# Optimization experiments

Hardware: AMD Instinct MI355X
Metric: run time of the kernel (lower is better)

The kernel has to match this reference:

```python
import jax, jax.numpy as jnp
import numpy as np

# SREChead (single level, width=0.25): stem 1x1 (128->64) + two 3x3 convs (64->64),
# each Conv->BN(eval, folded into scale/shift)->SiLU, then 1x1 reg (4ch) and obj (1ch)
# heads, followed by YOLOX-style grid decode.
B, C_IN, HGT, WID = 64, 128, 80, 80
C_H = 64            # int(256 * 0.25)
STRIDE = 32


def _conv(x, w):
    # NCHW conv, stride 1, SAME padding (pad=(k-1)//2 as in BaseConv)
    return jax.lax.conv_general_dilated(
        x, w, window_strides=(1, 1), padding='SAME',
        dimension_numbers=('NCHW', 'OIHW', 'NCHW'))


def _bn_silu(y, scale, shift):
    # eval-mode BatchNorm folded to per-channel affine, then SiLU
    return jax.nn.silu(y * scale[None, :, None, None] + shift[None, :, None, None])


def setup_inputs() -> dict:
    key = jax.random.key(0)
    ks = jax.random.split(key, 12)

    def w(k, o, i, kh, kw, s=0.05):
        return jax.random.normal(k, (o, i, kh, kw), jnp.float32) * s

    def bn(k, c):
        k1, k2 = jax.random.split(k)
        scale = 1.0 + 0.1 * jax.random.normal(k1, (c,), jnp.float32)
        shift = 0.05 * jax.random.normal(k2, (c,), jnp.float32)
        return scale, shift

    stem_scale, stem_shift = bn(ks[2], C_H)
    c1_scale, c1_shift = bn(ks[4], C_H)
    c2_scale, c2_shift = bn(ks[6], C_H)
    return {
        'x': jax.random.normal(ks[0], (B, C_IN, HGT, WID), jnp.float32),
        'stem_w': w(ks[1], C_H, C_IN, 1, 1),
        'stem_scale': stem_scale, 'stem_shift': stem_shift,
        'c1_w': w(ks[3], C_H, C_H, 3, 3),
        'c1_scale': c1_scale, 'c1_shift': c1_shift,
        'c2_w': w(ks[5], C_H, C_H, 3, 3),
        'c2_scale': c2_scale, 'c2_shift': c2_shift,
        'reg_w': w(ks[7], 4, C_H, 1, 1),
        'reg_b': jnp.zeros((4,), jnp.float32),
        'obj_w': w(ks[8], 1, C_H, 1, 1),
        'obj_b': jnp.zeros((1,), jnp.float32),
    }


def reference(x, stem_w, stem_scale, stem_shift,
              c1_w, c1_scale, c1_shift,
              c2_w, c2_scale, c2_shift,
              reg_w, reg_b, obj_w, obj_b):
    f = _bn_silu(_conv(x, stem_w), stem_scale, stem_shift)       # [B,64,H,W]
    f = _bn_silu(_conv(f, c1_w), c1_scale, c1_shift)
    f = _bn_silu(_conv(f, c2_w), c2_scale, c2_shift)
    reg = _conv(f, reg_w) + reg_b[None, :, None, None]           # [B,4,H,W]
    obj = jax.nn.sigmoid(_conv(f, obj_w) + obj_b[None, :, None, None])  # [B,1,H,W]
    out = jnp.concatenate([reg, obj], axis=1)                    # [B,5,H,W]
    out = out.reshape(out.shape[0], 5, HGT * WID).transpose(0, 2, 1)  # [B,HW,5]
    # YOLOX decode: xy = (pred_xy + grid) * stride, wh = exp(pred_wh) * stride
    yv, xv = jnp.meshgrid(jnp.arange(HGT), jnp.arange(WID), indexing='ij')
    grid = jnp.stack([xv, yv], -1).reshape(1, HGT * WID, 2).astype(out.dtype)
    xy = (out[..., :2] + grid) * STRIDE
    wh = jnp.exp(out[..., 2:4]) * STRIDE
    return jnp.concatenate([xy, wh, out[..., 4:5]], axis=-1)     # [B,HW,5]
```

## Files before the change

kernel.cpp:

```cpp
#include <hip/hip_runtime.h>
#include <cstdint>


typedef short short8 __attribute__((ext_vector_type(8)));
typedef float floatx4 __attribute__((ext_vector_type(4)));
typedef float fx4 __attribute__((ext_vector_type(4)));
typedef unsigned short us4 __attribute__((ext_vector_type(4)));

#define NPIX 6400
#define PADIMG (82 * 82 * 64)

static __device__ __forceinline__ unsigned short f2bf(float f) {
    unsigned u = __builtin_bit_cast(unsigned, f);
    u += 0x7fffu + ((u >> 16) & 1u);
    return (unsigned short)(u >> 16);
}

static __device__ __forceinline__ float silu_(float v) {
    return v / (1.0f + __expf(-v));
}

__global__ __launch_bounds__(256) void rearr_w_kernel(
    const float* __restrict__ w1, const float* __restrict__ w2,
    unsigned short* __restrict__ wB1, unsigned short* __restrict__ wB2) {
    int idx = blockIdx.x * 256 + threadIdx.x;
    const float* src = (idx < 36864) ? w1 : w2;
    unsigned short* dst = (idx < 36864) ? wB1 : wB2;
    int e = (idx < 36864) ? idx : idx - 36864;
    int j = e & 7;
    int lane = (e >> 3) & 63;
    int ct = (e >> 9) & 3;
    int kb = e >> 11;
    int co = ct * 16 + (lane & 15);
    int k = kb * 32 + ((lane >> 4) * 8) + j;
    int ci = k & 63;
    int tap = k >> 6;
    dst[e] = f2bf(src[(co * 64 + ci) * 9 + tap]);
}

__global__ __launch_bounds__(256) void border_kernel(
    unsigned short* __restrict__ f1p, unsigned short* __restrict__ f2p) {
    int t = blockIdx.x * 256 + threadIdx.x;
    int chunk = t % 5184;
    int bb = t / 5184;
    int buf = bb >> 6, b = bb & 63;
    int pix = chunk >> 4;
    int c4 = (chunk & 15) * 4;
    int row, col;
    if (pix < 82)       { row = 0;  col = pix; }
    else if (pix < 164) { row = 81; col = pix - 82; }
    else { int j = pix - 164; row = 1 + (j >> 1); col = (j & 1) * 81; }
    unsigned short* base = (buf ? f2p : f1p) + (size_t)b * PADIMG + (row * 82 + col) * 64 + c4;
    us4 z = {0, 0, 0, 0};
    *(us4*)base = z;
}

__global__ __launch_bounds__(256) void stem_kernel(
    const float* __restrict__ x, const float* __restrict__ w,
    const float* __restrict__ scale, const float* __restrict__ shift,
    unsigned short* __restrict__ f1p) {
    int b = blockIdx.y;
    int wv = threadIdx.x >> 6;
    int lane = threadIdx.x & 63;
    int l15 = lane & 15, q = lane >> 4;
    int pbase = blockIdx.x * 256 + wv * 64;

    short8 wf[4][4];
    #pragma unroll
    for (int ct = 0; ct < 4; ++ct) {
        int co = ct * 16 + l15;
        #pragma unroll
        for (int kb = 0; kb < 4; ++kb) {
            const float* wp = w + co * 128 + kb * 32 + q * 8;
            fx4 a = *(const fx4*)wp;
            fx4 bv = *(const fx4*)(wp + 4);
            short8 f;
            #pragma unroll
            for (int j = 0; j < 4; ++j) f[j] = (short)f2bf(a[j]);
            #pragma unroll
            for (int j = 0; j < 4; ++j) f[j + 4] = (short)f2bf(bv[j]);
            wf[ct][kb] = f;
        }
    }
    float sc[4][4], sh[4][4];
    #pragma unroll
    for (int ct = 0; ct < 4; ++ct)
        #pragma unroll
        for (int r = 0; r < 4; ++r) {
            sc[ct][r] = scale[ct * 16 + q * 4 + r];
            sh[ct][r] = shift[ct * 16 + q * 4 + r];
        }

    floatx4 acc[4][4];
    floatx4 zf = {0.0f, 0.0f, 0.0f, 0.0f};
    #pragma unroll
    for (int ct = 0; ct < 4; ++ct)
        #pragma unroll
        for (int pt = 0; pt < 4; ++pt) acc[ct][pt] = zf;

    #pragma unroll
    for (int kb = 0; kb < 4; ++kb) {
        short8 xf[4];
        #pragma unroll
        for (int pt = 0; pt < 4; ++pt) {
            int p = pbase + pt * 16 + l15;
            const float* xp = x + (size_t)(b * 128 + kb * 32 + q * 8) * NPIX + p;
            short8 f;
            #pragma unroll
            for (int j = 0; j < 8; ++j) f[j] = (short)f2bf(xp[j * NPIX]);
            xf[pt] = f;
        }
        #pragma unroll
        for (int ct = 0; ct < 4; ++ct)
            #pragma unroll
            for (int pt = 0; pt < 4; ++pt)
                acc[ct][pt] = __builtin_amdgcn_mfma_f32_16x16x32_bf16(
                    wf[ct][kb], xf[pt], acc[ct][pt], 0, 0, 0);
    }

    #pragma unroll
    for (int pt = 0; pt < 4; ++pt) {
        int p = pbase + pt * 16 + l15;
        int y = p / 80, xc = p % 80;
        unsigned short* dst = f1p + (size_t)b * PADIMG + ((y + 1) * 82 + (xc + 1)) * 64;
        #pragma unroll
        for (int ct = 0; ct < 4; ++ct) {
            us4 v;
            #pragma unroll
            for (int r = 0; r < 4; ++r)
                v[r] = f2bf(silu_(acc[ct][pt][r] * sc[ct][r] + sh[ct][r]));
            *(us4*)(dst + ct * 16 + q * 4) = v;
        }
    }
}

__global__ __launch_bounds__(256, 3) void conv3_kernel(
    const unsigned short* __restrict__ fin, const unsigned short* __restrict__ wB,
    const float* __restrict__ scale, const float* __restrict__ shift,
    unsigned short* __restrict__ fout) {
    int b = blockIdx.y;
    int wv = threadIdx.x >> 6;
    int lane = threadIdx.x & 63;
    int l15 = lane & 15, q = lane >> 4;
    int pbase = blockIdx.x * 256 + wv * 64;

    int py[4], px0[4];
    #pragma unroll
    for (int pt = 0; pt < 4; ++pt) {
        int pt16 = pbase + pt * 16;
        py[pt] = pt16 / 80;
        px0[pt] = pt16 % 80;
    }

    floatx4 acc[4][4];
    floatx4 zf = {0.0f, 0.0f, 0.0f, 0.0f};
    #pragma unroll
    for (int ct = 0; ct < 4; ++ct)
        #pragma unroll
        for (int pt = 0; pt < 4; ++pt) acc[ct][pt] = zf;

    const unsigned short* fb = fin + (size_t)b * PADIMG;

    #pragma unroll
    for (int tap = 0; tap < 9; ++tap) {
        const int dy = tap / 3 - 1, dx = tap % 3 - 1;
        #pragma unroll
        for (int half = 0; half < 2; ++half) {
            const int kb = tap * 2 + half;
            short8 pf[4];
            #pragma unroll
            for (int pt = 0; pt < 4; ++pt) {
                int addr = ((py[pt] + 1 + dy) * 82 + px0[pt] + l15 + 1 + dx) * 64
                         + half * 32 + q * 8;
                pf[pt] = *(const short8*)(fb + addr);
            }
            short8 wf[4];
            #pragma unroll
            for (int ct = 0; ct < 4; ++ct)
                wf[ct] = *(const short8*)(wB + ((kb * 4 + ct) * 64 + lane) * 8);
            #pragma unroll
            for (int ct = 0; ct < 4; ++ct)
                #pragma unroll
                for (int pt = 0; pt < 4; ++pt)
                    acc[ct][pt] = __builtin_amdgcn_mfma_f32_16x16x32_bf16(
                        wf[ct], pf[pt], acc[ct][pt], 0, 0, 0);
        }
    }

    float sc[4][4], sh[4][4];
    #pragma unroll
    for (int ct = 0; ct < 4; ++ct)
        #pragma unroll
        for (int r = 0; r < 4; ++r) {
            sc[ct][r] = scale[ct * 16 + q * 4 + r];
            sh[ct][r] = shift[ct * 16 + q * 4 + r];
        }
    #pragma unroll
    for (int pt = 0; pt < 4; ++pt) {
        unsigned short* dst = fout + (size_t)b * PADIMG
                            + ((py[pt] + 1) * 82 + px0[pt] + l15 + 1) * 64;
        #pragma unroll
        for (int ct = 0; ct < 4; ++ct) {
            us4 v;
            #pragma unroll
            for (int r = 0; r < 4; ++r)
                v[r] = f2bf(silu_(acc[ct][pt][r] * sc[ct][r] + sh[ct][r]));
            *(us4*)(dst + ct * 16 + q * 4) = v;
        }
    }
}

__global__ __launch_bounds__(256, 3) void conv_head_kernel(
    const unsigned short* __restrict__ fin, const unsigned short* __restrict__ wB,
    const float* __restrict__ scale, const float* __restrict__ shift,
    const float* __restrict__ reg_w, const float* __restrict__ reg_b,
    const float* __restrict__ obj_w, const float* __restrict__ obj_b,
    float* __restrict__ out) {
    __shared__ unsigned short h_lds[4][64 * 72];
    int b = blockIdx.y;
    int wv = threadIdx.x >> 6;
    int lane = threadIdx.x & 63;
    int l15 = lane & 15, q = lane >> 4;
    int pbase = blockIdx.x * 256 + wv * 64;

    int py[4], px0[4];
    #pragma unroll
    for (int pt = 0; pt < 4; ++pt) {
        int pt16 = pbase + pt * 16;
        py[pt] = pt16 / 80;
        px0[pt] = pt16 % 80;
    }

    floatx4 acc[4][4];
    floatx4 zf = {0.0f, 0.0f, 0.0f, 0.0f};
    #pragma unroll
    for (int ct = 0; ct < 4; ++ct)
        #pragma unroll
        for (int pt = 0; pt < 4; ++pt) acc[ct][pt] = zf;

    const unsigned short* fb = fin + (size_t)b * PADIMG;

    #pragma unroll
    for (int tap = 0; tap < 9; ++tap) {
        const int dy = tap / 3 - 1, dx = tap % 3 - 1;
        #pragma unroll
        for (int half = 0; half < 2; ++half) {
            const int kb = tap * 2 + half;
            short8 pf[4];
            #pragma unroll
            for (int pt = 0; pt < 4; ++pt) {
                int addr = ((py[pt] + 1 + dy) * 82 + px0[pt] + l15 + 1 + dx) * 64
                         + half * 32 + q * 8;
                pf[pt] = *(const short8*)(fb + addr);
            }
            short8 wf[4];
            #pragma unroll
            for (int ct = 0; ct < 4; ++ct)
                wf[ct] = *(const short8*)(wB + ((kb * 4 + ct) * 64 + lane) * 8);
            #pragma unroll
            for (int ct = 0; ct < 4; ++ct)
                #pragma unroll
                for (int pt = 0; pt < 4; ++pt)
                    acc[ct][pt] = __builtin_amdgcn_mfma_f32_16x16x32_bf16(
                        wf[ct], pf[pt], acc[ct][pt], 0, 0, 0);
        }
    }

    float sc[4][4], sh[4][4];
    #pragma unroll
    for (int ct = 0; ct < 4; ++ct)
        #pragma unroll
        for (int r = 0; r < 4; ++r) {
            sc[ct][r] = scale[ct * 16 + q * 4 + r];
            sh[ct][r] = shift[ct * 16 + q * 4 + r];
        }
    unsigned short* hp = h_lds[wv];
    #pragma unroll
    for (int pt = 0; pt < 4; ++pt) {
        #pragma unroll
        for (int ct = 0; ct < 4; ++ct) {
            us4 v;
            #pragma unroll
            for (int r = 0; r < 4; ++r)
                v[r] = f2bf(silu_(acc[ct][pt][r] * sc[ct][r] + sh[ct][r]));
            *(us4*)(hp + (pt * 16 + l15) * 72 + ct * 16 + q * 4) = v;
        }
    }
    __syncthreads();

    short8 hbf[2];
    #pragma unroll
    for (int kb2 = 0; kb2 < 2; ++kb2) {
        int k0 = kb2 * 32 + q * 8;
        short8 f = {};
        if (l15 < 4) {
            #pragma unroll
            for (int j = 0; j < 8; ++j) f[j] = (short)f2bf(reg_w[l15 * 64 + k0 + j]);
        } else if (l15 == 4) {
            #pragma unroll
            for (int j = 0; j < 8; ++j) f[j] = (short)f2bf(obj_w[k0 + j]);
        }
        hbf[kb2] = f;
    }

    floatx4 acc5[4];
    #pragma unroll
    for (int mt = 0; mt < 4; ++mt) acc5[mt] = zf;
    #pragma unroll
    for (int mt = 0; mt < 4; ++mt)
        #pragma unroll
        for (int kb2 = 0; kb2 < 2; ++kb2) {
            short8 a = *(const short8*)(hp + (mt * 16 + l15) * 72 + kb2 * 32 + q * 8);
            acc5[mt] = __builtin_amdgcn_mfma_f32_16x16x32_bf16(a, hbf[kb2], acc5[mt], 0, 0, 0);
        }

    float bias = 0.0f;
    if (l15 < 4) bias = reg_b[l15];
    else if (l15 == 4) bias = obj_b[0];

    #pragma unroll
    for (int mt = 0; mt < 4; ++mt) {
        #pragma unroll
        for (int r = 0; r < 4; ++r) {
            int p = pbase + mt * 16 + q * 4 + r;
            if (l15 < 5) {
                float v = acc5[mt][r] + bias;
                float gx = (float)(px0[mt] + q * 4 + r);
                float gy = (float)py[mt];
                float o;
                if (l15 == 0)      o = (v + gx) * 32.0f;
                else if (l15 == 1) o = (v + gy) * 32.0f;
                else if (l15 < 4)  o = __expf(v) * 32.0f;
                else               o = 1.0f / (1.0f + __expf(-v));
                out[(size_t)(b * NPIX + p) * 5 + l15] = o;
            }
        }
    }
}

extern "C" void kernel_launch(void* const* d_in, const int* in_sizes, int n_in,
                              void* d_out, int out_size, void* d_ws, size_t ws_size,
                              hipStream_t stream) {
    const float* x          = (const float*)d_in[0];
    const float* stem_w     = (const float*)d_in[1];
    const float* stem_scale = (const float*)d_in[2];
    const float* stem_shift = (const float*)d_in[3];
    const float* c1_w       = (const float*)d_in[4];
    const float* c1_scale   = (const float*)d_in[5];
    const float* c1_shift   = (const float*)d_in[6];
    const float* c2_w       = (const float*)d_in[7];
    const float* c2_scale   = (const float*)d_in[8];
    const float* c2_shift   = (const float*)d_in[9];
    const float* reg_w      = (const float*)d_in[10];
    const float* reg_b      = (const float*)d_in[11];
    const float* obj_w      = (const float*)d_in[12];
    const float* obj_b      = (const float*)d_in[13];
    float* out = (float*)d_out;

    const size_t needed = ((size_t)73728 + 2 * (size_t)64 * PADIMG) * 2;
    if (ws_size < needed) return;

    unsigned short* ws  = (unsigned short*)d_ws;
    unsigned short* wB1 = ws;
    unsigned short* wB2 = ws + 36864;
    unsigned short* f1p = ws + 73728;
    unsigned short* f2p = f1p + (size_t)64 * PADIMG;

    rearr_w_kernel<<<288, 256, 0, stream>>>(c1_w, c2_w, wB1, wB2);
    border_kernel<<<2592, 256, 0, stream>>>(f1p, f2p);
    stem_kernel<<<dim3(25, 64), 256, 0, stream>>>(x, stem_w, stem_scale, stem_shift, f1p);
    conv3_kernel<<<dim3(25, 64), 256, 0, stream>>>(f1p, wB1, c1_scale, c1_shift, f2p);
    conv_head_kernel<<<dim3(25, 64), 256, 0, stream>>>(f2p, wB2, c2_scale, c2_shift,
                                                       reg_w, reg_b, obj_w, obj_b, out);
}
```

Measured before the change: 543.1 us.

## Stage conv halo tiles in LDS, keep weights in registers, drop padded buffers

The 3x3 conv kernels now load a swizzled 6x82 pixel halo tile into shared memory once per block. Each wave holds one 16-channel output slice of weights in registers and loops over 20 pixel tiles, so global re-reads of neighbouring pixels are replaced by LDS reads. The padded intermediate layout and its border-zeroing kernel are removed, with out-of-bounds taps zero-filled during the tile load. The stem kernel now transposes its input through LDS to get coalesced fp32 loads. The costs are a large LDS footprint, more registers (launch bounds lowered to 2 blocks per SM) and a fixed 4-row tiling.

```diff
diff --git a/kernel.cpp b/kernel.cpp
--- a/kernel.cpp
+++ b/kernel.cpp
@@ -8,7 +8,6 @@
 typedef unsigned short us4 __attribute__((ext_vector_type(4)));
 
 #define NPIX 6400
-#define PADIMG (82 * 82 * 64)
 
 static __device__ __forceinline__ unsigned short f2bf(float f) {
     unsigned u = __builtin_bit_cast(unsigned, f);
@@ -38,32 +37,29 @@
     dst[e] = f2bf(src[(co * 64 + ci) * 9 + tap]);
 }
 
-__global__ __launch_bounds__(256) void border_kernel(
-    unsigned short* __restrict__ f1p, unsigned short* __restrict__ f2p) {
-    int t = blockIdx.x * 256 + threadIdx.x;
-    int chunk = t % 5184;
-    int bb = t / 5184;
-    int buf = bb >> 6, b = bb & 63;
-    int pix = chunk >> 4;
-    int c4 = (chunk & 15) * 4;
-    int row, col;
-    if (pix < 82)       { row = 0;  col = pix; }
-    else if (pix < 164) { row = 81; col = pix - 82; }
-    else { int j = pix - 164; row = 1 + (j >> 1); col = (j & 1) * 81; }
-    unsigned short* base = (buf ? f2p : f1p) + (size_t)b * PADIMG + (row * 82 + col) * 64 + c4;
-    us4 z = {0, 0, 0, 0};
-    *(us4*)base = z;
-}
-
 __global__ __launch_bounds__(256) void stem_kernel(
     const float* __restrict__ x, const float* __restrict__ w,
     const float* __restrict__ scale, const float* __restrict__ shift,
-    unsigned short* __restrict__ f1p) {
+    unsigned short* __restrict__ f1) {
+    __shared__ __align__(16) unsigned short xt[128 * 128];
     int b = blockIdx.y;
-    int wv = threadIdx.x >> 6;
-    int lane = threadIdx.x & 63;
+    int tid = threadIdx.x;
+    int pbase = blockIdx.x * 128;
+    int lane = tid & 63, wv = tid >> 6;
     int l15 = lane & 15, q = lane >> 4;
-    int pbase = blockIdx.x * 256 + wv * 64;
+
+    #pragma unroll
+    for (int i = 0; i < 16; ++i) {
+        int ci = i * 8 + (tid >> 5);
+        int pxq = tid & 31;
+        const float* xp = x + ((size_t)b * 128 + ci) * NPIX + pbase + pxq * 4;
+        fx4 v = *(const fx4*)xp;
+        #pragma unroll
+        for (int j = 0; j < 4; ++j) {
+            int px = pxq * 4 + j;
+            xt[px * 128 + (((ci >> 3) ^ (px & 15)) * 8) + (ci & 7)] = f2bf(v[j]);
+        }
+    }
 
     short8 wf[4][4];
     #pragma unroll
@@ -91,202 +87,197 @@
             sh[ct][r] = shift[ct * 16 + q * 4 + r];
         }
 
-    floatx4 acc[4][4];
+    __syncthreads();
+
+    floatx4 acc[4][2];
     floatx4 zf = {0.0f, 0.0f, 0.0f, 0.0f};
     #pragma unroll
     for (int ct = 0; ct < 4; ++ct)
         #pragma unroll
-        for (int pt = 0; pt < 4; ++pt) acc[ct][pt] = zf;
+        for (int t = 0; t < 2; ++t) acc[ct][t] = zf;
 
     #pragma unroll
     for (int kb = 0; kb < 4; ++kb) {
-        short8 xf[4];
-        #pragma unroll
-        for (int pt = 0; pt < 4; ++pt) {
-            int p = pbase + pt * 16 + l15;
-            const float* xp = x + (size_t)(b * 128 + kb * 32 + q * 8) * NPIX + p;
-            short8 f;
-            #pragma unroll
-            for (int j = 0; j < 8; ++j) f[j] = (short)f2bf(xp[j * NPIX]);
-            xf[pt] = f;
+        short8 xf[2];
+        #pragma unroll
+        for (int t = 0; t < 2; ++t) {
+            int px = (wv * 2 + t) * 16 + l15;
+            xf[t] = *(const short8*)(xt + px * 128 + (((kb * 4 + q) ^ (px & 15)) * 8));
         }
         #pragma unroll
         for (int ct = 0; ct < 4; ++ct)
             #pragma unroll
-            for (int pt = 0; pt < 4; ++pt)
-                acc[ct][pt] = __builtin_amdgcn_mfma_f32_16x16x32_bf16(
-                    wf[ct][kb], xf[pt], acc[ct][pt], 0, 0, 0);
-    }
-
-    #pragma unroll
-    for (int pt = 0; pt < 4; ++pt) {
-        int p = pbase + pt * 16 + l15;
-        int y = p / 80, xc = p % 80;
-        unsigned short* dst = f1p + (size_t)b * PADIMG + ((y + 1) * 82 + (xc + 1)) * 64;
+            for (int t = 0; t < 2; ++t)
+                acc[ct][t] = __builtin_amdgcn_mfma_f32_16x16x32_bf16(
+                    wf[ct][kb], xf[t], acc[ct][t], 0, 0, 0);
+    }
+
+    #pragma unroll
+    for (int t = 0; t < 2; ++t) {
+        int pg = pbase + (wv * 2 + t) * 16 + l15;
+        unsigned short* dst = f1 + ((size_t)b * NPIX + pg) * 64;
         #pragma unroll
         for (int ct = 0; ct < 4; ++ct) {
             us4 v;
             #pragma unroll
             for (int r = 0; r < 4; ++r)
-                v[r] = f2bf(silu_(acc[ct][pt][r] * sc[ct][r] + sh[ct][r]));
+                v[r] = f2bf(silu_(acc[ct][t][r] * sc[ct][r] + sh[ct][r]));
             *(us4*)(dst + ct * 16 + q * 4) = v;
         }
     }
 }
 
-__global__ __launch_bounds__(256, 3) void conv3_kernel(
+__global__ __launch_bounds__(256, 2) void conv3_kernel(
     const unsigned short* __restrict__ fin, const unsigned short* __restrict__ wB,
     const float* __restrict__ scale, const float* __restrict__ shift,
     unsigned short* __restrict__ fout) {
+    __shared__ __align__(16) unsigned short tile[492 * 64];
     int b = blockIdx.y;
-    int wv = threadIdx.x >> 6;
-    int lane = threadIdx.x & 63;
+    int y0 = blockIdx.x * 4;
+    int tid = threadIdx.x;
+    int lane = tid & 63, wv = tid >> 6;
     int l15 = lane & 15, q = lane >> 4;
-    int pbase = blockIdx.x * 256 + wv * 64;
-
-    int py[4], px0[4];
-    #pragma unroll
-    for (int pt = 0; pt < 4; ++pt) {
-        int pt16 = pbase + pt * 16;
-        py[pt] = pt16 / 80;
-        px0[pt] = pt16 % 80;
-    }
-
-    floatx4 acc[4][4];
+
+    const unsigned short* fb = fin + (size_t)b * NPIX * 64;
+    #pragma unroll
+    for (int i = 0; i < 16; ++i) {
+        int cid = i * 256 + tid;
+        if (cid < 3936) {
+            int pixL = cid >> 3, chunk = cid & 7;
+            int r = pixL / 82, c = pixL - r * 82;
+            int gy = y0 - 1 + r, gx = c - 1;
+            short8 v = {};
+            if ((unsigned)gy < 80u && (unsigned)gx < 80u)
+                v = *(const short8*)(fb + (size_t)(gy * 80 + gx) * 64 + chunk * 8);
+            *(short8*)(tile + pixL * 64 + ((chunk ^ (pixL & 7)) * 8)) = v;
+        }
+    }
+
+    short8 wreg[18];
+    #pragma unroll
+    for (int kb = 0; kb < 18; ++kb)
+        wreg[kb] = *(const short8*)(wB + ((kb * 4 + wv) * 64 + lane) * 8);
+
+    __syncthreads();
+
+    floatx4 acc[20];
     floatx4 zf = {0.0f, 0.0f, 0.0f, 0.0f};
     #pragma unroll
-    for (int ct = 0; ct < 4; ++ct)
-        #pragma unroll
-        for (int pt = 0; pt < 4; ++pt) acc[ct][pt] = zf;
-
-    const unsigned short* fb = fin + (size_t)b * PADIMG;
+    for (int pt = 0; pt < 20; ++pt) acc[pt] = zf;
 
     #pragma unroll
     for (int tap = 0; tap < 9; ++tap) {
         const int dy = tap / 3 - 1, dx = tap % 3 - 1;
         #pragma unroll
         for (int half = 0; half < 2; ++half) {
-            const int kb = tap * 2 + half;
-            short8 pf[4];
-            #pragma unroll
-            for (int pt = 0; pt < 4; ++pt) {
-                int addr = ((py[pt] + 1 + dy) * 82 + px0[pt] + l15 + 1 + dx) * 64
-                         + half * 32 + q * 8;
-                pf[pt] = *(const short8*)(fb + addr);
+            short8 w8 = wreg[tap * 2 + half];
+            #pragma unroll
+            for (int pt = 0; pt < 20; ++pt) {
+                const int r_o = pt / 5, c_o = (pt % 5) * 16;
+                int pix = (r_o + 1 + dy) * 82 + c_o + l15 + 1 + dx;
+                short8 bf8 = *(const short8*)(
+                    tile + pix * 64 + (((half * 4 + q) ^ (pix & 7)) * 8));
+                acc[pt] = __builtin_amdgcn_mfma_f32_16x16x32_bf16(
+                    w8, bf8, acc[pt], 0, 0, 0);
             }
-            short8 wf[4];
-            #pragma unroll
-            for (int ct = 0; ct < 4; ++ct)
-                wf[ct] = *(const short8*)(wB + ((kb * 4 + ct) * 64 + lane) * 8);
-            #pragma unroll
-            for (int ct = 0; ct < 4; ++ct)
-                #pragma unroll
-                for (int pt = 0; pt < 4; ++pt)
-                    acc[ct][pt] = __builtin_amdgcn_mfma_f32_16x16x32_bf16(
-                        wf[ct], pf[pt], acc[ct][pt], 0, 0, 0);
-        }
-    }
-
-    float sc[4][4], sh[4][4];
-    #pragma unroll
-    for (int ct = 0; ct < 4; ++ct)
-        #pragma unroll
-        for (int r = 0; r < 4; ++r) {
-            sc[ct][r] = scale[ct * 16 + q * 4 + r];
-            sh[ct][r] = shift[ct * 16 + q * 4 + r];
-        }
-    #pragma unroll
-    for (int pt = 0; pt < 4; ++pt) {
-        unsigned short* dst = fout + (size_t)b * PADIMG
-                            + ((py[pt] + 1) * 82 + px0[pt] + l15 + 1) * 64;
-        #pragma unroll
-        for (int ct = 0; ct < 4; ++ct) {
-            us4 v;
-            #pragma unroll
-            for (int r = 0; r < 4; ++r)
-                v[r] = f2bf(silu_(acc[ct][pt][r] * sc[ct][r] + sh[ct][r]));
-            *(us4*)(dst + ct * 16 + q * 4) = v;
-        }
-    }
-}
-
-__global__ __launch_bounds__(256, 3) void conv_head_kernel(
+        }
+    }
+
+    float sc4[4], sh4[4];
+    #pragma unroll
+    for (int r = 0; r < 4; ++r) {
+        sc4[r] = scale[wv * 16 + q * 4 + r];
+        sh4[r] = shift[wv * 16 + q * 4 + r];
+    }
+    #pragma unroll
+    for (int pt = 0; pt < 20; ++pt) {
+        const int r_o = pt / 5, c_o = (pt % 5) * 16;
+        int pg = (y0 + r_o) * 80 + c_o + l15;
+        us4 v;
+        #pragma unroll
+        for (int r = 0; r < 4; ++r)
+            v[r] = f2bf(silu_(acc[pt][r] * sc4[r] + sh4[r]));
+        *(us4*)(fout + ((size_t)b * NPIX + pg) * 64 + wv * 16 + q * 4) = v;
+    }
+}
+
+__global__ __launch_bounds__(256, 2) void conv_head_kernel(
     const unsigned short* __restrict__ fin, const unsigned short* __restrict__ wB,
     const float* __restrict__ scale, const float* __restrict__ shift,
     const float* __restrict__ reg_w, const float* __restrict__ reg_b,
     const float* __restrict__ obj_w, const float* __restrict__ obj_b,
     float* __restrict__ out) {
-    __shared__ unsigned short h_lds[4][64 * 72];
+    __shared__ __align__(16) unsigned short tile[492 * 64];
     int b = blockIdx.y;
-    int wv = threadIdx.x >> 6;
-    int lane = threadIdx.x & 63;
+    int y0 = blockIdx.x * 4;
+    int tid = threadIdx.x;
+    int lane = tid & 63, wv = tid >> 6;
     int l15 = lane & 15, q = lane >> 4;
-    int pbase = blockIdx.x * 256 + wv * 64;
-
-    int py[4], px0[4];
-    #pragma unroll
-    for (int pt = 0; pt < 4; ++pt) {
-        int pt16 = pbase + pt * 16;
-        py[pt] = pt16 / 80;
-        px0[pt] = pt16 % 80;
-    }
-
-    floatx4 acc[4][4];
+
+    const unsigned short* fb = fin + (size_t)b * NPIX * 64;
+    #pragma unroll
+    for (int i = 0; i < 16; ++i) {
+        int cid = i * 256 + tid;
+        if (cid < 3936) {
+            int pixL = cid >> 3, chunk = cid & 7;
+            int r = pixL / 82, c = pixL - r * 82;
+            int gy = y0 - 1 + r, gx = c - 1;
+            short8 v = {};
+            if ((unsigned)gy < 80u && (unsigned)gx < 80u)
+                v = *(const short8*)(fb + (size_t)(gy * 80 + gx) * 64 + chunk * 8);
+            *(short8*)(tile + pixL * 64 + ((chunk ^ (pixL & 7)) * 8)) = v;
+        }
+    }
+
+    short8 wreg[18];
+    #pragma unroll
+    for (int kb = 0; kb < 18; ++kb)
+        wreg[kb] = *(const short8*)(wB + ((kb * 4 + wv) * 64 + lane) * 8);
+
+    __syncthreads();
+
+    floatx4 acc[20];
     floatx4 zf = {0.0f, 0.0f, 0.0f, 0.0f};
     #pragma unroll
-    for (int ct = 0; ct < 4; ++ct)
-        #pragma unroll
-        for (int pt = 0; pt < 4; ++pt) acc[ct][pt] = zf;
-
-    const unsigned short* fb = fin + (size_t)b * PADIMG;
+    for (int pt = 0; pt < 20; ++pt) acc[pt] = zf;
 
     #pragma unroll
     for (int tap = 0; tap < 9; ++tap) {
         const int dy = tap / 3 - 1, dx = tap % 3 - 1;
         #pragma unroll
         for (int half = 0; half < 2; ++half) {
-            const int kb = tap * 2 + half;
-            short8 pf[4];
-            #pragma unroll
-            for (int pt = 0; pt < 4; ++pt) {
-                int addr = ((py[pt] + 1 + dy) * 82 + px0[pt] + l15 + 1 + dx) * 64
-                         + half * 32 + q * 8;
-                pf[pt] = *(const short8*)(fb + addr);
+            short8 w8 = wreg[tap * 2 + half];
+            #pragma unroll
+            for (int pt = 0; pt < 20; ++pt) {
+                const int r_o = pt / 5, c_o = (pt % 5) * 16;
+                int pix = (r_o + 1 + dy) * 82 + c_o + l15 + 1 + dx;
+                short8 bf8 = *(const short8*)(
+                    tile + pix * 64 + (((half * 4 + q) ^ (pix & 7)) * 8));
+                acc[pt] = __builtin_amdgcn_mfma_f32_16x16x32_bf16(
+                    w8, bf8, acc[pt], 0, 0, 0);
             }
-            short8 wf[4];
-            #pragma unroll
-            for (int ct = 0; ct < 4; ++ct)
-                wf[ct] = *(const short8*)(wB + ((kb * 4 + ct) * 64 + lane) * 8);
-            #pragma unroll
-            for (int ct = 0; ct < 4; ++ct)
-                #pragma unroll
-                for (int pt = 0; pt < 4; ++pt)
-                    acc[ct][pt] = __builtin_amdgcn_mfma_f32_16x16x32_bf16(
-                        wf[ct], pf[pt], acc[ct][pt], 0, 0, 0);
-        }
-    }
-
-    float sc[4][4], sh[4][4];
-    #pragma unroll
-    for (int ct = 0; ct < 4; ++ct)
-        #pragma unroll
-        for (int r = 0; r < 4; ++r) {
-            sc[ct][r] = scale[ct * 16 + q * 4 + r];
-            sh[ct][r] = shift[ct * 16 + q * 4 + r];
-        }
-    unsigned short* hp = h_lds[wv];
-    #pragma unroll
-    for (int pt = 0; pt < 4; ++pt) {
-        #pragma unroll
-        for (int ct = 0; ct < 4; ++ct) {
-            us4 v;
-            #pragma unroll
-            for (int r = 0; r < 4; ++r)
-                v[r] = f2bf(silu_(acc[ct][pt][r] * sc[ct][r] + sh[ct][r]));
-            *(us4*)(hp + (pt * 16 + l15) * 72 + ct * 16 + q * 4) = v;
-        }
-    }
-    __syncthreads();
+        }
+    }
+
+    __syncthreads();
+
+    float sc4[4], sh4[4];
+    #pragma unroll
+    for (int r = 0; r < 4; ++r) {
+        sc4[r] = scale[wv * 16 + q * 4 + r];
+        sh4[r] = shift[wv * 16 + q * 4 + r];
+    }
+    int gco = (wv * 2 + (q >> 1));
+    #pragma unroll
+    for (int pt = 0; pt < 20; ++pt) {
+        const int r_o = pt / 5, c_o = (pt % 5) * 16;
+        int pix = r_o * 80 + c_o + l15;
+        us4 v;
+        #pragma unroll
+        for (int r = 0; r < 4; ++r)
+            v[r] = f2bf(silu_(acc[pt][r] * sc4[r] + sh4[r]));
+        *(us4*)(tile + pix * 64 + ((gco ^ (pix & 7)) * 8) + (q & 1) * 4) = v;
+    }
 
     short8 hbf[2];
     #pragma unroll
@@ -303,36 +294,44 @@
         hbf[kb2] = f;
     }
 
-    floatx4 acc5[4];
-    #pragma unroll
-    for (int mt = 0; mt < 4; ++mt) acc5[mt] = zf;
-    #pragma unroll
-    for (int mt = 0; mt < 4; ++mt)
+    __syncthreads();
+
+    floatx4 acc5[5];
+    #pragma unroll
+    for (int t = 0; t < 5; ++t) acc5[t] = zf;
+    #pragma unroll
+    for (int t = 0; t < 5; ++t) {
+        int mt = wv * 5 + t;
         #pragma unroll
         for (int kb2 = 0; kb2 < 2; ++kb2) {
-            short8 a = *(const short8*)(hp + (mt * 16 + l15) * 72 + kb2 * 32 + q * 8);
-            acc5[mt] = __builtin_amdgcn_mfma_f32_16x16x32_bf16(a, hbf[kb2], acc5[mt], 0, 0, 0);
-        }
+            int pix = mt * 16 + l15;
+            short8 a = *(const short8*)(
+                tile + pix * 64 + (((kb2 * 4 + q) ^ (pix & 7)) * 8));
+            acc5[t] = __builtin_amdgcn_mfma_f32_16x16x32_bf16(
+                a, hbf[kb2], acc5[t], 0, 0, 0);
+        }
+    }
 
     float bias = 0.0f;
     if (l15 < 4) bias = reg_b[l15];
     else if (l15 == 4) bias = obj_b[0];
 
     #pragma unroll
-    for (int mt = 0; mt < 4; ++mt) {
+    for (int t = 0; t < 5; ++t) {
+        int mt = wv * 5 + t;
         #pragma unroll
         for (int r = 0; r < 4; ++r) {
-            int p = pbase + mt * 16 + q * 4 + r;
+            int pixL = mt * 16 + q * 4 + r;
             if (l15 < 5) {
-                float v = acc5[mt][r] + bias;
-                float gx = (float)(px0[mt] + q * 4 + r);
-                float gy = (float)py[mt];
+                float v = acc5[t][r] + bias;
+                float gx = (float)(pixL % 80);
+                float gy = (float)(y0 + pixL / 80);
                 float o;
                 if (l15 == 0)      o = (v + gx) * 32.0f;
                 else if (l15 == 1) o = (v + gy) * 32.0f;
                 else if (l15 < 4)  o = __expf(v) * 32.0f;
                 else               o = 1.0f / (1.0f + __expf(-v));
-                out[(size_t)(b * NPIX + p) * 5 + l15] = o;
+                out[((size_t)b * NPIX + y0 * 80 + pixL) * 5 + l15] = o;
             }
         }
     }
@@ -357,19 +356,18 @@
     const float* obj_b      = (const float*)d_in[13];
     float* out = (float*)d_out;
 
-    const size_t needed = ((size_t)73728 + 2 * (size_t)64 * PADIMG) * 2;
+    const size_t needed = ((size_t)73728 + 2 * (size_t)64 * NPIX * 64) * 2;
     if (ws_size < needed) return;
 
     unsigned short* ws  = (unsigned short*)d_ws;
     unsigned short* wB1 = ws;
     unsigned short* wB2 = ws + 36864;
-    unsigned short* f1p = ws + 73728;
-    unsigned short* f2p = f1p + (size_t)64 * PADIMG;
+    unsigned short* f1  = ws + 73728;
+    unsigned short* f2  = f1 + (size_t)64 * NPIX * 64;
 
     rearr_w_kernel<<<288, 256, 0, stream>>>(c1_w, c2_w, wB1, wB2);
-    border_kernel<<<2592, 256, 0, stream>>>(f1p, f2p);
-    stem_kernel<<<dim3(25, 64), 256, 0, stream>>>(x, stem_w, stem_scale, stem_shift, f1p);
-    conv3_kernel<<<dim3(25, 64), 256, 0, stream>>>(f1p, wB1, c1_scale, c1_shift, f2p);
-    conv_head_kernel<<<dim3(25, 64), 256, 0, stream>>>(f2p, wB2, c2_scale, c2_shift,
+    stem_kernel<<<dim3(50, 64), 256, 0, stream>>>(x, stem_w, stem_scale, stem_shift, f1);
+    conv3_kernel<<<dim3(20, 64), 256, 0, stream>>>(f1, wB1, c1_scale, c1_shift, f2);
+    conv_head_kernel<<<dim3(20, 64), 256, 0, stream>>>(f2, wB2, c2_scale, c2_shift,
                                                        reg_w, reg_b, obj_w, obj_b, out);
 }
```

New measurement: 840.9 us. 54.8% more time.
